# Performance work log

Hardware: AMD Instinct MI355X
Metric: run time of the kernel (lower is better)

## Reference

```python
import jax, jax.numpy as jnp
import numpy as np

B, LS, VS = 4, 1024, 1024
VH, LH, H = 1024, 1024, 16
HD = LH // H  # head_dim = 64


def setup_inputs() -> dict:
    key = jax.random.key(0)
    ks = jax.random.split(key, 10)
    s = 0.02
    return {
        "v_hidden_states": jax.random.normal(ks[0], (B, VS, VH), jnp.float32),
        "l_hidden_states": jax.random.normal(ks[1], (B, LS, LH), jnp.float32),
        "q_w": jax.random.normal(ks[2], (LH, LH), jnp.float32) * s,
        "q_b": jnp.zeros((LH,), jnp.float32),
        "k_w": jax.random.normal(ks[3], (VH, LH), jnp.float32) * s,
        "k_b": jnp.zeros((LH,), jnp.float32),
        "v_w": jax.random.normal(ks[4], (VH, LH), jnp.float32) * s,
        "v_b": jnp.zeros((LH,), jnp.float32),
        "o_w": jax.random.normal(ks[5], (LH, LH), jnp.float32) * s,
        "o_b": jnp.zeros((LH,), jnp.float32),
    }


def reference(v_hidden_states, l_hidden_states, q_w, q_b, k_w, k_b, v_w, v_b, o_w, o_b):
    b, ls, _ = l_hidden_states.shape
    vs = v_hidden_states.shape[1]
    q = (l_hidden_states @ q_w + q_b).reshape(b, ls, H, HD)
    k = (v_hidden_states @ k_w + k_b).reshape(b, vs, H, HD)
    v = (v_hidden_states @ v_w + v_b).reshape(b, vs, H, HD)
    # NOTE: original scales by sqrt(hidden_size), not sqrt(head_dim)
    scale = jnp.sqrt(jnp.asarray(LH, q.dtype))
    scores = jnp.einsum("blhd,bvhd->bhlv", q, k) / scale
    attn = jax.nn.softmax(scores, axis=-1)
    out = jnp.einsum("bhlv,bvhd->blhd", attn, v).reshape(b, ls, LH)
    return out @ o_w + o_b
```

## Files before the change

kernel.cpp:

```cpp
#include <hip/hip_runtime.h>

typedef __bf16 bf16;
typedef __attribute__((ext_vector_type(4))) __bf16 bf16x4;
typedef __attribute__((ext_vector_type(8))) __bf16 bf16x8;
typedef __attribute__((ext_vector_type(4))) float f32x4;

static __device__ __forceinline__ f32x4 mfma_16x16x32(bf16x8 a, bf16x8 b, f32x4 c) {
    return __builtin_amdgcn_mfma_f32_16x16x32_bf16(a, b, c, 0, 0, 0);
}

static __device__ __forceinline__ bf16x8 load8(const float* p) {
    f32x4 a = *(const f32x4*)p;
    f32x4 b = *(const f32x4*)(p + 4);
    bf16x8 r;
    r[0] = (bf16)a[0]; r[1] = (bf16)a[1]; r[2] = (bf16)a[2]; r[3] = (bf16)a[3];
    r[4] = (bf16)b[0]; r[5] = (bf16)b[1]; r[6] = (bf16)b[2]; r[7] = (bf16)b[3];
    return r;
}

static __device__ __forceinline__ void gload_lds16(const void* g, void* l) {
    __builtin_amdgcn_global_load_lds(
        (const __attribute__((address_space(1))) void*)g,
        (__attribute__((address_space(3))) void*)l, 16, 0, 0);
}

#define QSCALE 0.0450842200277801f

#define SYNC_PRE(N)                                                      \
    do {                                                                 \
        asm volatile("s_waitcnt vmcnt(" #N ")" ::: "memory");            \
        __builtin_amdgcn_s_barrier();                                    \
        __builtin_amdgcn_sched_barrier(0);                               \
    } while (0)

#define SYNC_POST()                                                     \
    do {                                                                \
        asm volatile("s_waitcnt lgkmcnt(0)" ::: "memory");              \
        __builtin_amdgcn_sched_barrier(0);                              \
        __builtin_amdgcn_s_barrier();                                   \
    } while (0)

__global__ __launch_bounds__(256) void prep_kernel(
    const float* __restrict__ l_h, const float* __restrict__ v_h,
    const float* __restrict__ w0, const float* __restrict__ w1,
    const float* __restrict__ w2, const float* __restrict__ w3,
    bf16* __restrict__ l_bf, bf16* __restrict__ v_bf,
    bf16* __restrict__ dq, bf16* __restrict__ dkv, bf16* __restrict__ dov)
{
    const int id = blockIdx.x;
    if (id < 4096) {
        const float* s = (id < 2048) ? l_h : v_h;
        bf16*       d = (id < 2048) ? l_bf : v_bf;
        const int   bb = (id < 2048) ? id : id - 2048;
        const size_t i = ((size_t)bb * 256 + threadIdx.x) * 8;
        *(bf16x8*)(d + i) = load8(s + i);
        return;
    }
    const int widx = id - 4096;
    const int z    = widx >> 8;
    const int rem  = widx & 255;
    const int j0   = (rem & 15) * 64;
    const int i0   = (rem >> 4) * 64;
    const float* src; bf16* dst;
    switch (z) {
        case 0:  src = w0; dst = dq; break;
        case 1:  src = w1; dst = dkv; break;
        case 2:  src = w2; dst = dkv + (size_t)1024 * 1024; break;
        default: src = w3; dst = dov; break;
    }
    const float wscale = (z == 0) ? QSCALE : 1.0f;
    __shared__ float T[64][65];
    const int tx = threadIdx.x & 15;
    const int ty = threadIdx.x >> 4;
    #pragma unroll
    for (int it = 0; it < 4; ++it) {
        f32x4 v = *(const f32x4*)(src + (size_t)(i0 + ty + it * 16) * 1024 + j0 + tx * 4);
        T[ty + it * 16][tx * 4 + 0] = v[0];
        T[ty + it * 16][tx * 4 + 1] = v[1];
        T[ty + it * 16][tx * 4 + 2] = v[2];
        T[ty + it * 16][tx * 4 + 3] = v[3];
    }
    __syncthreads();
    #pragma unroll
    for (int it = 0; it < 4; ++it) {
        const int jj = ty + it * 16;
        bf16x4 o;
        o[0] = (bf16)(T[tx * 4 + 0][jj] * wscale);
        o[1] = (bf16)(T[tx * 4 + 1][jj] * wscale);
        o[2] = (bf16)(T[tx * 4 + 2][jj] * wscale);
        o[3] = (bf16)(T[tx * 4 + 3][jj] * wscale);
        *(bf16x4*)(dst + (size_t)(j0 + jj) * 1024 + i0 + tx * 4) = o;
    }
}

__global__ __launch_bounds__(256, 3) void proj128_kernel(
    const bf16* __restrict__ l_bf, const bf16* __restrict__ v_bf,
    const bf16* __restrict__ QWt,  const bf16* __restrict__ KVWt,
    const float* __restrict__ q_b, const float* __restrict__ k_b,
    const float* __restrict__ v_b,
    bf16* __restrict__ Qh, bf16* __restrict__ Kh, bf16* __restrict__ Vt)
{
    __shared__ __align__(16) bf16 As[3][128][32];
    __shared__ __align__(16) bf16 Bs[3][128][32];

    const int t    = threadIdx.x;
    const int lane = t & 63;
    const int wave = t >> 6;
    const int wm   = wave & 1;
    const int wn   = wave >> 1;
    const int l15  = lane & 15;
    const int quad = lane >> 4;

    const int orig = blockIdx.y * 24 + blockIdx.x;
    const int wg   = (orig & 7) * 96 + (orig >> 3);
    const int by   = wg / 24;
    const int bx   = wg - by * 24;

    const bool isQ = bx < 8;
    const bf16* A  = isQ ? l_bf : v_bf;
    const bf16* Bt = isQ ? QWt  : KVWt;
    const int  gn0 = (isQ ? bx : bx - 8) * 128;
    const int  gm0 = by * 128;
    const int  K   = 1024;

    const int srow    = lane >> 2;
    const int chunk_g = (lane & 3) ^ ((srow >> 1) & 3);
    const size_t aoff = (size_t)(gm0 + wave * 32 + srow) * K + chunk_g * 8;
    const size_t boff = (size_t)(gn0 + wave * 32 + srow) * K + chunk_g * 8;

    f32x4 acc[4][4];
    #pragma unroll
    for (int i = 0; i < 4; ++i)
        #pragma unroll
        for (int j = 0; j < 4; ++j)
            acc[i][j] = (f32x4){0.f, 0.f, 0.f, 0.f};

    #define PSTAGE(k0_, buf_)                                                      \
        {                                                                          \
            _Pragma("unroll")                                                      \
            for (int q = 0; q < 2; ++q) {                                          \
                gload_lds16(A  + aoff + (size_t)q * 16 * K + (k0_),                \
                            &As[buf_][wave * 32 + q * 16][0]);                     \
                gload_lds16(Bt + boff + (size_t)q * 16 * K + (k0_),                \
                            &Bs[buf_][wave * 32 + q * 16][0]);                     \
            }                                                                      \
        }

    #define PCOMPUTE(bufi)                                                         \
        {                                                                          \
            bf16x8 af[4], bfr[4];                                                  \
            _Pragma("unroll")                                                      \
            for (int mt = 0; mt < 4; ++mt) {                                       \
                const int row = wm * 64 + mt * 16 + l15;                           \
                af[mt] = *(const bf16x8*)(&As[bufi][row][(quad ^ ((row >> 1) & 3)) * 8]); \
            }                                                                      \
            _Pragma("unroll")                                                      \
            for (int nt = 0; nt < 4; ++nt) {                                       \
                const int row = wn * 64 + nt * 16 + l15;                           \
                bfr[nt] = *(const bf16x8*)(&Bs[bufi][row][(quad ^ ((row >> 1) & 3)) * 8]); \
            }                                                                      \
            __builtin_amdgcn_s_setprio(1);                                         \
            _Pragma("unroll")                                                      \
            for (int mt = 0; mt < 4; ++mt)                                         \
                _Pragma("unroll")                                                  \
                for (int nt = 0; nt < 4; ++nt)                                     \
                    acc[mt][nt] = mfma_16x16x32(af[mt], bfr[nt], acc[mt][nt]);     \
            __builtin_amdgcn_s_setprio(0);                                         \
        }

    PSTAGE(0, 0);
    PSTAGE(32, 1);
    int bc = 0, bn2 = 2;

    for (int k0 = 0; k0 < K - 64; k0 += 32) {
        PSTAGE(k0 + 64, bn2);
        SYNC_PRE(8);
        PCOMPUTE(bc);
        SYNC_POST();
        int nb = bc + 1;  if (nb == 3) nb = 0;
        int nn = bn2 + 1; if (nn == 3) nn = 0;
        bc = nb; bn2 = nn;
    }
    SYNC_PRE(4);
    PCOMPUTE(bc);
    SYNC_POST();
    bc = (bc + 1 == 3) ? 0 : bc + 1;
    SYNC_PRE(0);
    PCOMPUTE(bc);

    #undef PSTAGE
    #undef PCOMPUTE

    #pragma unroll
    for (int nt = 0; nt < 4; ++nt) {
        const int col = gn0 + wn * 64 + nt * 16 + l15;
        float bb; bf16* dst; bool hm;
        if (isQ)             { bb = q_b[col] * QSCALE;   dst = Qh; hm = true;  }
        else if (col < 1024) { bb = k_b[col];            dst = Kh; hm = true;  }
        else                 { bb = v_b[col - 1024];     dst = Vt; hm = false; }
        #pragma unroll
        for (int mt = 0; mt < 4; ++mt) {
            #pragma unroll
            for (int r = 0; r < 4; ++r) {
                const int row = gm0 + wm * 64 + mt * 16 + quad * 4 + r;
                const float v = acc[mt][nt][r] + bb;
                if (hm) {
                    const size_t idx =
                        ((size_t)((row >> 10) * 16 + (col >> 6)) * 1024 +
                         (row & 1023)) * 64 + (col & 63);
                    dst[idx] = (bf16)v;
                } else {
                    const int vc = col - 1024;
                    const size_t idx =
                        ((size_t)((row >> 10) * 16 + (vc >> 6)) * 64 +
                         (vc & 63)) * 1024 + (row & 1023);
                    dst[idx] = (bf16)v;
                }
            }
        }
    }
}

__global__ __launch_bounds__(256, 3) void ogemm_kernel(
    const bf16* __restrict__ Aw, const bf16* __restrict__ OWt,
    const float* __restrict__ o_b, float* __restrict__ C)
{
    __shared__ __align__(16) bf16 As[3][128][32];
    __shared__ __align__(16) bf16 Bs[3][64][32];

    const int t    = threadIdx.x;
    const int lane = t & 63;
    const int wave = t >> 6;
    const int wm   = wave & 1;
    const int wn   = wave >> 1;
    const int l15  = lane & 15;
    const int quad = lane >> 4;

    const int orig = blockIdx.y * 16 + blockIdx.x;
    const int wg   = (orig & 7) * 64 + (orig >> 3);
    const int by   = wg >> 4;
    const int bx   = wg & 15;

    const int gn0 = bx * 64;
    const int gm0 = by * 128;
    const int K   = 1024;

    const int srow    = lane >> 2;
    const int chunk_g = (lane & 3) ^ ((srow >> 1) & 3);
    const size_t aoff = (size_t)(gm0 + wave * 32 + srow) * K + chunk_g * 8;
    const size_t boff = (size_t)(gn0 + wave * 16 + srow) * K + chunk_g * 8;

    f32x4 acc[4][2];
    #pragma unroll
    for (int i = 0; i < 4; ++i)
        #pragma unroll
        for (int j = 0; j < 2; ++j)
            acc[i][j] = (f32x4){0.f, 0.f, 0.f, 0.f};

    #define OSTAGE(k0_, buf_)                                                          \
        {                                                                              \
            gload_lds16(Aw + aoff + (k0_),                  &As[buf_][wave * 32][0]);  \
            gload_lds16(Aw + aoff + (size_t)16 * K + (k0_), &As[buf_][wave * 32 + 16][0]); \
            gload_lds16(OWt + boff + (k0_),                 &Bs[buf_][wave * 16][0]);  \
        }

    #define OCOMPUTE(bufi)                                                             \
        {                                                                              \
            bf16x8 af[4], bfr[2];                                                      \
            _Pragma("unroll")                                                          \
            for (int mt = 0; mt < 4; ++mt) {                                           \
                const int row = wm * 64 + mt * 16 + l15;                               \
                af[mt] = *(const bf16x8*)(&As[bufi][row][(quad ^ ((row >> 1) & 3)) * 8]); \
            }                                                                          \
            _Pragma("unroll")                                                          \
            for (int nt = 0; nt < 2; ++nt) {                                           \
                const int row = wn * 32 + nt * 16 + l15;                               \
                bfr[nt] = *(const bf16x8*)(&Bs[bufi][row][(quad ^ ((row >> 1) & 3)) * 8]); \
            }                                                                          \
            __builtin_amdgcn_s_setprio(1);                                             \
            _Pragma("unroll")                                                          \
            for (int mt = 0; mt < 4; ++mt)                                             \
                _Pragma("unroll")                                                      \
                for (int nt = 0; nt < 2; ++nt)                                         \
                    acc[mt][nt] = mfma_16x16x32(af[mt], bfr[nt], acc[mt][nt]);         \
            __builtin_amdgcn_s_setprio(0);                                             \
        }

    OSTAGE(0, 0);
    OSTAGE(32, 1);
    int bc = 0, bn2 = 2;

    for (int k0 = 0; k0 < K - 64; k0 += 32) {
        OSTAGE(k0 + 64, bn2);
        SYNC_PRE(6);
        OCOMPUTE(bc);
        SYNC_POST();
        int nb = bc + 1;  if (nb == 3) nb = 0;
        int nn = bn2 + 1; if (nn == 3) nn = 0;
        bc = nb; bn2 = nn;
    }
    SYNC_PRE(3);
    OCOMPUTE(bc);
    SYNC_POST();
    bc = (bc + 1 == 3) ? 0 : bc + 1;
    SYNC_PRE(0);
    OCOMPUTE(bc);

    #undef OSTAGE
    #undef OCOMPUTE

    #pragma unroll
    for (int nt = 0; nt < 2; ++nt) {
        const int col = gn0 + wn * 32 + nt * 16 + l15;
        const float bb = o_b[col];
        #pragma unroll
        for (int mt = 0; mt < 4; ++mt) {
            #pragma unroll
            for (int r = 0; r < 4; ++r) {
                const int row = gm0 + wm * 64 + mt * 16 + quad * 4 + r;
                C[(size_t)row * 1024 + col] = acc[mt][nt][r] + bb;
            }
        }
    }
}

__global__ __launch_bounds__(256) void attn_kernel(
    const bf16* __restrict__ Q, const bf16* __restrict__ K,
    const bf16* __restrict__ V, bf16* __restrict__ O)
{
    const int t    = threadIdx.x;
    const int lane = t & 63;
    const int wave = t >> 6;
    const int l15  = lane & 15;
    const int quad = lane >> 4;

    const int head = blockIdx.x;
    const int q0   = blockIdx.y * 128;
    const int b    = head >> 4;
    const int h    = head & 15;

    __shared__ __align__(16) bf16 Kb[2][64][64];
    __shared__ __align__(16) bf16 Vb[2][64][64];
    __shared__ __align__(16) bf16 P[4][32][72];

    const bf16* Qp  = Q + ((size_t)head * 1024 + q0 + wave * 32) * 64;
    const bf16* Kp  = K + (size_t)head * 1024 * 64;
    const bf16* Vtp = V + (size_t)head * 64 * 1024;

    const int r8  = lane >> 3;
    const int c8  = lane & 7;
    const int swz = (c8 ^ r8) * 8;

    bf16x8 aq[2][2];
    #pragma unroll
    for (int mt = 0; mt < 2; ++mt)
        #pragma unroll
        for (int kc = 0; kc < 2; ++kc)
            aq[mt][kc] = *(const bf16x8*)(Qp + (mt * 16 + l15) * 64 + kc * 32 + quad * 8);

    bf16x8 vones;
    #pragma unroll
    for (int j = 0; j < 8; ++j) vones[j] = (bf16)1.0f;

    f32x4 oacc[2][4];
    #pragma unroll
    for (int mt = 0; mt < 2; ++mt)
        #pragma unroll
        for (int nt = 0; nt < 4; ++nt)
            oacc[mt][nt] = (f32x4){0.f, 0.f, 0.f, 0.f};
    f32x4 lacc[2];
    lacc[0] = (f32x4){0.f, 0.f, 0.f, 0.f};
    lacc[1] = (f32x4){0.f, 0.f, 0.f, 0.f};

    #define STAGE(c, buf)                                                          \
        {                                                                          \
            const int kv0_ = (c) * 64;                                             \
            _Pragma("unroll")                                                      \
            for (int g = 0; g < 2; ++g) {                                          \
                const int R = wave * 16 + g * 8;                                   \
                gload_lds16(Kp + (size_t)(kv0_ + R + r8) * 64 + swz,               \
                            &Kb[buf][R][0]);                                       \
                gload_lds16(Vtp + (size_t)(R + r8) * 1024 + kv0_ + swz,            \
                            &Vb[buf][R][0]);                                       \
            }                                                                      \
        }

    STAGE(0, 0);

    const int sw = l15 & 7;

    for (int c = 0; c < 16; ++c) {
        const int buf = c & 1;
        __syncthreads();
        if (c + 1 < 16) STAGE(c + 1, buf ^ 1);

        #pragma unroll
        for (int nt = 0; nt < 4; ++nt) {
            const bf16* krow = &Kb[buf][nt * 16 + l15][0];
            bf16x8 bk0 = *(const bf16x8*)(krow + (quad ^ sw) * 8);
            bf16x8 bk1 = *(const bf16x8*)(krow + ((quad + 4) ^ sw) * 8);
            #pragma unroll
            for (int mt = 0; mt < 2; ++mt) {
                f32x4 s = (f32x4){0.f, 0.f, 0.f, 0.f};
                s = mfma_16x16x32(aq[mt][0], bk0, s);
                s = mfma_16x16x32(aq[mt][1], bk1, s);
                #pragma unroll
                for (int r = 0; r < 4; ++r) {
                    const float e = __builtin_amdgcn_exp2f(s[r]);
                    P[wave][mt * 16 + quad * 4 + r][nt * 16 + l15] = (bf16)e;
                }
            }
        }

        #pragma unroll
        for (int mt = 0; mt < 2; ++mt) {
            bf16x8 pa0 = *(const bf16x8*)(&P[wave][mt * 16 + l15][quad * 8]);
            bf16x8 pa1 = *(const bf16x8*)(&P[wave][mt * 16 + l15][32 + quad * 8]);
            lacc[mt] = mfma_16x16x32(pa0, vones, lacc[mt]);
            lacc[mt] = mfma_16x16x32(pa1, vones, lacc[mt]);
            #pragma unroll
            for (int nt = 0; nt < 4; ++nt) {
                const bf16* vrow = &Vb[buf][nt * 16 + l15][0];
                bf16x8 bv0 = *(const bf16x8*)(vrow + (quad ^ sw) * 8);
                bf16x8 bv1 = *(const bf16x8*)(vrow + ((quad + 4) ^ sw) * 8);
                oacc[mt][nt] = mfma_16x16x32(pa0, bv0, oacc[mt][nt]);
                oacc[mt][nt] = mfma_16x16x32(pa1, bv1, oacc[mt][nt]);
            }
        }
    }
    #undef STAGE

    #pragma unroll
    for (int mt = 0; mt < 2; ++mt) {
        const float invs[4] = {1.0f / lacc[mt][0], 1.0f / lacc[mt][1],
                               1.0f / lacc[mt][2], 1.0f / lacc[mt][3]};
        #pragma unroll
        for (int nt = 0; nt < 4; ++nt) {
            #pragma unroll
            for (int r = 0; r < 4; ++r) {
                const int row = q0 + wave * 32 + mt * 16 + quad * 4 + r;
                O[((size_t)b * 1024 + row) * 1024 + h * 64 + nt * 16 + l15] =
                    (bf16)(oacc[mt][nt][r] * invs[r]);
            }
        }
    }
}

extern "C" void kernel_launch(void* const* d_in, const int* in_sizes, int n_in,
                              void* d_out, int out_size, void* d_ws, size_t ws_size,
                              hipStream_t stream)
{
    const float* v_h = (const float*)d_in[0];
    const float* l_h = (const float*)d_in[1];
    const float* q_w = (const float*)d_in[2];
    const float* q_b = (const float*)d_in[3];
    const float* k_w = (const float*)d_in[4];
    const float* k_b = (const float*)d_in[5];
    const float* v_w = (const float*)d_in[6];
    const float* v_b = (const float*)d_in[7];
    const float* o_w = (const float*)d_in[8];
    const float* o_b = (const float*)d_in[9];
    float* out = (float*)d_out;

    const size_t SZ = (size_t)4096 * 1024;
    const size_t WZ = (size_t)1024 * 1024;

    bf16* l_bf = (bf16*)d_ws;
    bf16* v_bf = l_bf + SZ;
    bf16* QWt  = v_bf + SZ;
    bf16* KVWt = QWt + WZ;
    bf16* OWt  = KVWt + 2 * WZ;
    bf16* Qh   = OWt + WZ;
    bf16* Kh   = Qh + SZ;
    bf16* Vt   = Kh + SZ;
    bf16* Aw   = Vt + SZ;

    prep_kernel<<<dim3(5120), 256, 0, stream>>>(
        l_h, v_h, q_w, k_w, v_w, o_w, l_bf, v_bf, QWt, KVWt, OWt);

    proj128_kernel<<<dim3(24, 32), 256, 0, stream>>>(
        l_bf, v_bf, QWt, KVWt, q_b, k_b, v_b, Qh, Kh, Vt);

    attn_kernel<<<dim3(64, 8), 256, 0, stream>>>(Qh, Kh, Vt, Aw);

    ogemm_kernel<<<dim3(16, 32), 256, 0, stream>>>(Aw, OWt, o_b, out);

    (void)in_sizes; (void)n_in; (void)out_size; (void)ws_size;
}
```

Measured before the change: 189.8 us.

## Retile projection GEMM to 256x256 tiles with 8 waves and 64-wide K stages

Replaces the 128x128, 4-wave projection GEMM (triple-buffered, K-step 32) with a 256x256 tile using 512 threads, a K-step of 64 and double-buffered LDS with an XOR swizzle. Larger tiles are meant to raise arithmetic intensity and halve the number of pipeline iterations and barriers. In exchange, the grid shrinks to 192 workgroups, which may leave CUs idle. Per-thread accumulator register pressure also doubles, which may limit latency hiding.

```diff
diff --git a/kernel.cpp b/kernel.cpp
--- a/kernel.cpp
+++ b/kernel.cpp
@@ -93,15 +93,15 @@
     }
 }
 
-__global__ __launch_bounds__(256, 3) void proj128_kernel(
+__global__ __launch_bounds__(512, 2) void proj256_kernel(
     const bf16* __restrict__ l_bf, const bf16* __restrict__ v_bf,
     const bf16* __restrict__ QWt,  const bf16* __restrict__ KVWt,
     const float* __restrict__ q_b, const float* __restrict__ k_b,
     const float* __restrict__ v_b,
     bf16* __restrict__ Qh, bf16* __restrict__ Kh, bf16* __restrict__ Vt)
 {
-    __shared__ __align__(16) bf16 As[3][128][32];
-    __shared__ __align__(16) bf16 Bs[3][128][32];
+    __shared__ __align__(16) bf16 Asl[2][256][64];
+    __shared__ __align__(16) bf16 Bsl[2][256][64];
 
     const int t    = threadIdx.x;
     const int lane = t & 63;
@@ -110,86 +110,105 @@
     const int wn   = wave >> 1;
     const int l15  = lane & 15;
     const int quad = lane >> 4;
-
-    const int orig = blockIdx.y * 24 + blockIdx.x;
-    const int wg   = (orig & 7) * 96 + (orig >> 3);
-    const int by   = wg / 24;
-    const int bx   = wg - by * 24;
-
-    const bool isQ = bx < 8;
-    const bf16* A  = isQ ? l_bf : v_bf;
+    const int swz  = l15 & 7;
+
+    const int orig = blockIdx.x;
+    const int wg   = (orig & 7) * 24 + (orig >> 3);
+    const int by   = wg / 12;
+    const int bx   = wg - by * 12;
+
+    const bool isQ = bx < 4;
+    const bf16* Ap = isQ ? l_bf : v_bf;
     const bf16* Bt = isQ ? QWt  : KVWt;
-    const int  gn0 = (isQ ? bx : bx - 8) * 128;
-    const int  gm0 = by * 128;
-    const int  K   = 1024;
-
-    const int srow    = lane >> 2;
-    const int chunk_g = (lane & 3) ^ ((srow >> 1) & 3);
-    const size_t aoff = (size_t)(gm0 + wave * 32 + srow) * K + chunk_g * 8;
-    const size_t boff = (size_t)(gn0 + wave * 32 + srow) * K + chunk_g * 8;
-
-    f32x4 acc[4][4];
-    #pragma unroll
-    for (int i = 0; i < 4; ++i)
+    const int  gn0 = (isQ ? bx : bx - 4) * 256;
+    const int  gm0 = by * 256;
+
+    const int srow8 = t >> 3;
+    const int gch   = (t & 7) ^ (srow8 & 7);
+    const size_t abase = (size_t)(gm0 + srow8) * 1024 + gch * 8;
+    const size_t bbase = (size_t)(gn0 + srow8) * 1024 + gch * 8;
+
+    f32x4 acc[8][4];
+    #pragma unroll
+    for (int i = 0; i < 8; ++i)
         #pragma unroll
         for (int j = 0; j < 4; ++j)
             acc[i][j] = (f32x4){0.f, 0.f, 0.f, 0.f};
 
-    #define PSTAGE(k0_, buf_)                                                      \
+    #define STG(kt_, b_)                                                           \
         {                                                                          \
             _Pragma("unroll")                                                      \
-            for (int q = 0; q < 2; ++q) {                                          \
-                gload_lds16(A  + aoff + (size_t)q * 16 * K + (k0_),                \
-                            &As[buf_][wave * 32 + q * 16][0]);                     \
-                gload_lds16(Bt + boff + (size_t)q * 16 * K + (k0_),                \
-                            &Bs[buf_][wave * 32 + q * 16][0]);                     \
-            }                                                                      \
-        }
-
-    #define PCOMPUTE(bufi)                                                         \
+            for (int q = 0; q < 4; ++q)                                            \
+                gload_lds16(Ap + abase + (size_t)q * 64 * 1024 + (kt_) * 64,       \
+                            &Asl[b_][q * 64 + wave * 8][0]);                       \
+            _Pragma("unroll")                                                      \
+            for (int q = 0; q < 4; ++q)                                            \
+                gload_lds16(Bt + bbase + (size_t)q * 64 * 1024 + (kt_) * 64,       \
+                            &Bsl[b_][q * 64 + wave * 8][0]);                       \
+        }
+
+    #define CTILE(b_)                                                              \
         {                                                                          \
-            bf16x8 af[4], bfr[4];                                                  \
-            _Pragma("unroll")                                                      \
-            for (int mt = 0; mt < 4; ++mt) {                                       \
-                const int row = wm * 64 + mt * 16 + l15;                           \
-                af[mt] = *(const bf16x8*)(&As[bufi][row][(quad ^ ((row >> 1) & 3)) * 8]); \
-            }                                                                      \
-            _Pragma("unroll")                                                      \
-            for (int nt = 0; nt < 4; ++nt) {                                       \
-                const int row = wn * 64 + nt * 16 + l15;                           \
-                bfr[nt] = *(const bf16x8*)(&Bs[bufi][row][(quad ^ ((row >> 1) & 3)) * 8]); \
-            }                                                                      \
+            bf16x8 bfv[4][2], af[4][2];                                            \
+            _Pragma("unroll")                                                      \
+            for (int nt = 0; nt < 4; ++nt)                                         \
+                _Pragma("unroll")                                                  \
+                for (int kk = 0; kk < 2; ++kk)                                     \
+                    bfv[nt][kk] = *(const bf16x8*)(&Bsl[b_][wn * 64 + nt * 16 + l15] \
+                                                        [((kk * 4 + quad) ^ swz) * 8]); \
+            _Pragma("unroll")                                                      \
+            for (int i = 0; i < 4; ++i)                                            \
+                _Pragma("unroll")                                                  \
+                for (int kk = 0; kk < 2; ++kk)                                     \
+                    af[i][kk] = *(const bf16x8*)(&Asl[b_][wm * 128 + i * 16 + l15] \
+                                                      [((kk * 4 + quad) ^ swz) * 8]); \
             __builtin_amdgcn_s_setprio(1);                                         \
             _Pragma("unroll")                                                      \
-            for (int mt = 0; mt < 4; ++mt)                                         \
+            for (int i = 0; i < 4; ++i)                                            \
                 _Pragma("unroll")                                                  \
                 for (int nt = 0; nt < 4; ++nt)                                     \
-                    acc[mt][nt] = mfma_16x16x32(af[mt], bfr[nt], acc[mt][nt]);     \
+                    _Pragma("unroll")                                              \
+                    for (int kk = 0; kk < 2; ++kk)                                 \
+                        acc[i][nt] = mfma_16x16x32(af[i][kk], bfv[nt][kk], acc[i][nt]); \
             __builtin_amdgcn_s_setprio(0);                                         \
-        }
-
-    PSTAGE(0, 0);
-    PSTAGE(32, 1);
-    int bc = 0, bn2 = 2;
-
-    for (int k0 = 0; k0 < K - 64; k0 += 32) {
-        PSTAGE(k0 + 64, bn2);
-        SYNC_PRE(8);
-        PCOMPUTE(bc);
-        SYNC_POST();
-        int nb = bc + 1;  if (nb == 3) nb = 0;
-        int nn = bn2 + 1; if (nn == 3) nn = 0;
-        bc = nb; bn2 = nn;
-    }
-    SYNC_PRE(4);
-    PCOMPUTE(bc);
-    SYNC_POST();
-    bc = (bc + 1 == 3) ? 0 : bc + 1;
-    SYNC_PRE(0);
-    PCOMPUTE(bc);
-
-    #undef PSTAGE
-    #undef PCOMPUTE
+            _Pragma("unroll")                                                      \
+            for (int i = 0; i < 4; ++i)                                            \
+                _Pragma("unroll")                                                  \
+                for (int kk = 0; kk < 2; ++kk)                                     \
+                    af[i][kk] = *(const bf16x8*)(&Asl[b_][wm * 128 + 64 + i * 16 + l15] \
+                                                      [((kk * 4 + quad) ^ swz) * 8]); \
+            __builtin_amdgcn_s_setprio(1);                                         \
+            _Pragma("unroll")                                                      \
+            for (int i = 0; i < 4; ++i)                                            \
+                _Pragma("unroll")                                                  \
+                for (int nt = 0; nt < 4; ++nt)                                     \
+                    _Pragma("unroll")                                              \
+                    for (int kk = 0; kk < 2; ++kk)                                 \
+                        acc[4 + i][nt] = mfma_16x16x32(af[i][kk], bfv[nt][kk], acc[4 + i][nt]); \
+            __builtin_amdgcn_s_setprio(0);                                         \
+        }
+
+    STG(0, 0);
+    STG(1, 1);
+    asm volatile("s_waitcnt vmcnt(8)" ::: "memory");
+    __builtin_amdgcn_s_barrier();
+
+    for (int tt = 0; tt < 14; ++tt) {
+        const int b = tt & 1;
+        CTILE(b);
+        __builtin_amdgcn_s_barrier();
+        STG(tt + 2, b);
+        asm volatile("s_waitcnt vmcnt(8)" ::: "memory");
+        __builtin_amdgcn_s_barrier();
+    }
+    CTILE(0);
+    __builtin_amdgcn_s_barrier();
+    asm volatile("s_waitcnt vmcnt(0)" ::: "memory");
+    __builtin_amdgcn_s_barrier();
+    CTILE(1);
+
+    #undef STG
+    #undef CTILE
 
     #pragma unroll
     for (int nt = 0; nt < 4; ++nt) {
@@ -199,10 +218,10 @@
         else if (col < 1024) { bb = k_b[col];            dst = Kh; hm = true;  }
         else                 { bb = v_b[col - 1024];     dst = Vt; hm = false; }
         #pragma unroll
-        for (int mt = 0; mt < 4; ++mt) {
+        for (int mt = 0; mt < 8; ++mt) {
             #pragma unroll
             for (int r = 0; r < 4; ++r) {
-                const int row = gm0 + wm * 64 + mt * 16 + quad * 4 + r;
+                const int row = gm0 + wm * 128 + mt * 16 + quad * 4 + r;
                 const float v = acc[mt][nt][r] + bb;
                 if (hm) {
                     const size_t idx =
@@ -478,7 +497,7 @@
     prep_kernel<<<dim3(5120), 256, 0, stream>>>(
         l_h, v_h, q_w, k_w, v_w, o_w, l_bf, v_bf, QWt, KVWt, OWt);
 
-    proj128_kernel<<<dim3(24, 32), 256, 0, stream>>>(
+    proj256_kernel<<<dim3(192), 512, 0, stream>>>(
         l_bf, v_bf, QWt, KVWt, q_b, k_b, v_b, Qh, Kh, Vt);
 
     attn_kernel<<<dim3(64, 8), 256, 0, stream>>>(Qh, Kh, Vt, Aw);
```

After: 212.0 us. +11.7%, slower.

## Read K and V directly from global memory instead of LDS staging

Applied to the files above, without the earlier changes.

Removes the double-buffered LDS staging of K and V tiles, together with the per-iteration block barrier. Each wave now loads its K and V MFMA operands straight from global memory, relying on L1/L2 caching, and the loop is unrolled by two. This drops the syncthreads and async LDS copies, and lowers LDS use, which may raise occupancy. In exchange, the four waves each fetch the same K/V data redundantly through the cache, and global-load latency is exposed without explicit prefetching.

```diff
diff --git a/kernel.cpp b/kernel.cpp
--- a/kernel.cpp
+++ b/kernel.cpp
@@ -339,17 +339,11 @@
     const int b    = head >> 4;
     const int h    = head & 15;
 
-    __shared__ __align__(16) bf16 Kb[2][64][64];
-    __shared__ __align__(16) bf16 Vb[2][64][64];
     __shared__ __align__(16) bf16 P[4][32][72];
 
     const bf16* Qp  = Q + ((size_t)head * 1024 + q0 + wave * 32) * 64;
     const bf16* Kp  = K + (size_t)head * 1024 * 64;
     const bf16* Vtp = V + (size_t)head * 64 * 1024;
-
-    const int r8  = lane >> 3;
-    const int c8  = lane & 7;
-    const int swz = (c8 ^ r8) * 8;
 
     bf16x8 aq[2][2];
     #pragma unroll
@@ -372,33 +366,15 @@
     lacc[0] = (f32x4){0.f, 0.f, 0.f, 0.f};
     lacc[1] = (f32x4){0.f, 0.f, 0.f, 0.f};
 
-    #define STAGE(c, buf)                                                          \
-        {                                                                          \
-            const int kv0_ = (c) * 64;                                             \
-            _Pragma("unroll")                                                      \
-            for (int g = 0; g < 2; ++g) {                                          \
-                const int R = wave * 16 + g * 8;                                   \
-                gload_lds16(Kp + (size_t)(kv0_ + R + r8) * 64 + swz,               \
-                            &Kb[buf][R][0]);                                       \
-                gload_lds16(Vtp + (size_t)(R + r8) * 1024 + kv0_ + swz,            \
-                            &Vb[buf][R][0]);                                       \
-            }                                                                      \
-        }
-
-    STAGE(0, 0);
-
-    const int sw = l15 & 7;
-
+    #pragma unroll 2
     for (int c = 0; c < 16; ++c) {
-        const int buf = c & 1;
-        __syncthreads();
-        if (c + 1 < 16) STAGE(c + 1, buf ^ 1);
+        const int kv0 = c * 64;
 
         #pragma unroll
         for (int nt = 0; nt < 4; ++nt) {
-            const bf16* krow = &Kb[buf][nt * 16 + l15][0];
-            bf16x8 bk0 = *(const bf16x8*)(krow + (quad ^ sw) * 8);
-            bf16x8 bk1 = *(const bf16x8*)(krow + ((quad + 4) ^ sw) * 8);
+            const bf16* krow = Kp + (size_t)(kv0 + nt * 16 + l15) * 64;
+            bf16x8 bk0 = *(const bf16x8*)(krow + quad * 8);
+            bf16x8 bk1 = *(const bf16x8*)(krow + 32 + quad * 8);
             #pragma unroll
             for (int mt = 0; mt < 2; ++mt) {
                 f32x4 s = (f32x4){0.f, 0.f, 0.f, 0.f};
@@ -420,15 +396,14 @@
             lacc[mt] = mfma_16x16x32(pa1, vones, lacc[mt]);
             #pragma unroll
             for (int nt = 0; nt < 4; ++nt) {
-                const bf16* vrow = &Vb[buf][nt * 16 + l15][0];
-                bf16x8 bv0 = *(const bf16x8*)(vrow + (quad ^ sw) * 8);
-                bf16x8 bv1 = *(const bf16x8*)(vrow + ((quad + 4) ^ sw) * 8);
+                const bf16* vrow = Vtp + (size_t)(nt * 16 + l15) * 1024 + kv0;
+                bf16x8 bv0 = *(const bf16x8*)(vrow + quad * 8);
+                bf16x8 bv1 = *(const bf16x8*)(vrow + 32 + quad * 8);
                 oacc[mt][nt] = mfma_16x16x32(pa0, bv0, oacc[mt][nt]);
                 oacc[mt][nt] = mfma_16x16x32(pa1, bv1, oacc[mt][nt]);
             }
         }
     }
-    #undef STAGE
 
     #pragma unroll
     for (int mt = 0; mt < 2; ++mt) {
```

After: 222.8 us. +17.4%, slower.
